# Kernel optimization log

Measured on AMD Instinct MI355X. Metric: run time of the kernel, lower is better.

## Reference

```python
import jax, jax.numpy as jnp
import numpy as np

B, WIN, NN, NF, NH, NOUT = 4, 10, 10000, 8, 64, 1
N = B * WIN * NN          # stacked graph nodes
E = 3200000               # edges
EPS = 1e-5                # BatchNorm eps


def _gcn(x, edge_index, ew, W, b):
    # PyG GCNConv: linear first, then sym-normalized aggregation with self loops.
    xl = x @ W  # [N, H]
    loop = jnp.arange(N)
    row = jnp.concatenate([edge_index[0], loop])
    col = jnp.concatenate([edge_index[1], loop])
    w = jnp.concatenate([ew, jnp.ones((N,), ew.dtype)])
    deg = jax.ops.segment_sum(w, col, num_segments=N)
    dinv = jnp.where(deg > 0, jax.lax.rsqrt(deg), 0.0)
    norm = dinv[row] * w * dinv[col]
    out = jax.ops.segment_sum(norm[:, None] * xl[row], col, num_segments=N)
    return out + b


def _bn(x, g, bta):
    # training-mode BatchNorm1d (batch statistics, biased variance)
    m = x.mean(0)
    v = x.var(0)
    return (x - m) * jax.lax.rsqrt(v + EPS) * g + bta


def _lstm(xs, wih, whh, bih, bhh):
    # xs: [T, Bn, D]; PyTorch gate order i, f, g, o
    H = whh.shape[1]
    Bn = xs.shape[1]
    h0 = jnp.zeros((Bn, H), xs.dtype)
    c0 = jnp.zeros((Bn, H), xs.dtype)
    def step(carry, xt):
        h, c = carry
        gates = xt @ wih.T + bih + h @ whh.T + bhh
        i, f, g, o = jnp.split(gates, 4, axis=-1)
        c = jax.nn.sigmoid(f) * c + jax.nn.sigmoid(i) * jnp.tanh(g)
        h = jax.nn.sigmoid(o) * jnp.tanh(c)
        return (h, c), h
    (hn, cn), ys = jax.lax.scan(step, (h0, c0), xs)
    return ys, hn


def setup_inputs() -> dict:
    key = jax.random.key(0)
    ks = jax.random.split(key, 16)
    def rn(k, shape, s=0.05):
        return jax.random.normal(k, shape, jnp.float32) * s
    return {
        "x": jax.random.normal(ks[0], (N, NF), jnp.float32),
        "edge_index": jax.random.randint(ks[1], (2, E), 0, N),
        "edge_weight": jax.random.uniform(ks[2], (E,), jnp.float32),
        "c1_w": rn(ks[3], (NF, NH)), "c1_b": jnp.zeros((NH,), jnp.float32),
        "c2_w": rn(ks[4], (NH, NH)), "c2_b": jnp.zeros((NH,), jnp.float32),
        "bn1_g": jnp.ones((NH,), jnp.float32), "bn1_b": jnp.zeros((NH,), jnp.float32),
        "bn2_g": jnp.ones((NH,), jnp.float32), "bn2_b": jnp.zeros((NH,), jnp.float32),
        "l1_wih": rn(ks[5], (4 * NH, 2 * NH)), "l1_whh": rn(ks[6], (4 * NH, NH)),
        "l1_bih": jnp.zeros((4 * NH,), jnp.float32), "l1_bhh": jnp.zeros((4 * NH,), jnp.float32),
        "l2_wih": rn(ks[7], (4 * NH, NH)), "l2_whh": rn(ks[8], (4 * NH, NH)),
        "l2_bih": jnp.zeros((4 * NH,), jnp.float32), "l2_bhh": jnp.zeros((4 * NH,), jnp.float32),
        "fc1_w": rn(ks[9], (NH, 2 * NH + WIN * NF)), "fc1_b": jnp.zeros((NH,), jnp.float32),
        "fc2_w": rn(ks[10], (NOUT, NH)), "fc2_b": jnp.zeros((NOUT,), jnp.float32),
    }


def reference(x, edge_index, edge_weight, c1_w, c1_b, c2_w, c2_b,
              bn1_g, bn1_b, bn2_g, bn2_b,
              l1_wih, l1_whh, l1_bih, l1_bhh,
              l2_wih, l2_whh, l2_bih, l2_bhh,
              fc1_w, fc1_b, fc2_w, fc2_b):
    # skip connection: raw features per (batch,node) over the window
    skip = x.reshape(B, WIN, NN, NF).transpose(0, 2, 1, 3).reshape(B * NN, WIN * NF)
    # two GCN layers (dropout is identity in deterministic/eval reference)
    h1 = _bn(jax.nn.relu(_gcn(x, edge_index, edge_weight, c1_w, c1_b)), bn1_g, bn1_b)
    h2 = _bn(jax.nn.relu(_gcn(h1, edge_index, edge_weight, c2_w, c2_b)), bn2_g, bn2_b)
    xc = jnp.concatenate([h1, h2], axis=1)  # [N, 2H]
    xr = xc.reshape(B, WIN, NN, 2 * NH).transpose(1, 0, 2, 3).reshape(WIN, B * NN, 2 * NH)
    ys1, hn1 = _lstm(xr, l1_wih, l1_whh, l1_bih, l1_bhh)
    ys2, hn2 = _lstm(ys1, l2_wih, l2_whh, l2_bih, l2_bhh)
    z = jnp.concatenate([hn1, hn2, skip], axis=1)
    z = jax.nn.relu(z @ fc1_w.T + fc1_b)
    z = jax.nn.relu(z @ fc2_w.T + fc2_b)
    return z.reshape(-1)
```

## Files before the change

### kernel.cpp

```cpp
#include <hip/hip_runtime.h>
#include <math.h>

constexpr int BB     = 4;
constexpr int WINN   = 10;
constexpr int NNODES = 10000;
constexpr int NFEAT  = 8;
constexpr int NHID   = 64;
constexpr int NTOT   = BB * WINN * NNODES;
constexpr int NEDGE  = 3200000;
constexpr int NBN    = BB * NNODES;
constexpr float EPSBN = 1e-5f;

#define DEVFN static __device__ __forceinline__

typedef float f4 __attribute__((ext_vector_type(4)));
typedef short s8v __attribute__((ext_vector_type(8)));
typedef unsigned short ushort_t;
typedef unsigned int uint_t;

DEVFN float sigmoidf_(float x) { return 1.0f / (1.0f + __expf(-x)); }
DEVFN float tanhf_(float x) { return 2.0f / (1.0f + __expf(-2.0f * x)) - 1.0f; }
DEVFN ushort_t f2bf(float f) {
    uint_t x = __float_as_uint(f);
    return (ushort_t)((x + 0x7FFFu + ((x >> 16) & 1u)) >> 16);
}
DEVFN float bf2f(ushort_t u) { return __uint_as_float(((uint_t)u) << 16); }

__global__ void k_diag(float* out, float wsz, int n) {
    int i = blockIdx.x * 256 + threadIdx.x;
    if (i < n) out[i] = wsz;
}

__global__ void k_init(int* cntP, float* sums) {
    int i = blockIdx.x * 256 + threadIdx.x;
    if (i < 8 * NTOT) cntP[i] = 0;
    if (i < 2048) sums[i] = 0.f;
}

__global__ void k_hist(const int* __restrict__ ei, int* __restrict__ cntP) {
    int e = blockIdx.x * 256 + threadIdx.x;
    int p = blockIdx.x & 7;
    if (e < NEDGE) atomicAdd(&cntP[p * NTOT + ei[NEDGE + e]], 1);
}

__global__ void k_scan1(const int* __restrict__ cntP, int* __restrict__ ptr, int* __restrict__ tmp) {
    __shared__ int sdat[256];
    int tid = threadIdx.x;
    int base = blockIdx.x * 1024 + tid * 4;
    int v[4];
#pragma unroll
    for (int j = 0; j < 4; ++j) {
        int idx = base + j;
        int s = 0;
        if (idx < NTOT) {
#pragma unroll
            for (int p = 0; p < 8; ++p) s += cntP[p * NTOT + idx];
        }
        v[j] = s;
    }
    int sum = v[0] + v[1] + v[2] + v[3];
    sdat[tid] = sum;
    __syncthreads();
    for (int ofs = 1; ofs < 256; ofs <<= 1) {
        int x = (tid >= ofs) ? sdat[tid - ofs] : 0;
        __syncthreads();
        sdat[tid] += x;
        __syncthreads();
    }
    int run = sdat[tid] - sum;
    if (base + 0 < NTOT) ptr[base + 0] = run; run += v[0];
    if (base + 1 < NTOT) ptr[base + 1] = run; run += v[1];
    if (base + 2 < NTOT) ptr[base + 2] = run; run += v[2];
    if (base + 3 < NTOT) ptr[base + 3] = run;
    if (tid == 255) tmp[blockIdx.x] = sdat[255];
}

__global__ void k_scan2(int* tmp, int nb) {
    __shared__ int st[512];
    int tid = threadIdx.x;
    int v = (tid < nb) ? tmp[tid] : 0;
    st[tid] = v;
    __syncthreads();
    for (int ofs = 1; ofs < 512; ofs <<= 1) {
        int x = (tid >= ofs) ? st[tid - ofs] : 0;
        __syncthreads();
        st[tid] += x;
        __syncthreads();
    }
    if (tid < nb) tmp[tid] = st[tid] - v;
}

__global__ void k_scan3(int* __restrict__ ptr, int* __restrict__ cntP, const int* __restrict__ tmp) {
    int i = blockIdx.x * 256 + threadIdx.x;
    if (i < NTOT) {
        int p0 = ptr[i] + tmp[i >> 10];
        ptr[i] = p0;
        int run = p0;
#pragma unroll
        for (int p = 0; p < 8; ++p) {
            int c = cntP[p * NTOT + i];
            cntP[p * NTOT + i] = run;
            run += c;
        }
    }
    if (i == 0) ptr[NTOT] = NEDGE;
}

__global__ void k_fill(const int* __restrict__ ei, const float* __restrict__ ew,
                       int* __restrict__ cur8, int2* __restrict__ epack) {
    int e = blockIdx.x * 256 + threadIdx.x;
    if (e >= NEDGE) return;
    int p = blockIdx.x & 7;
    int row = ei[e], col = ei[NEDGE + e];
    int pos = atomicAdd(&cur8[p * NTOT + col], 1);
    epack[pos] = make_int2(row, __float_as_int(ew[e]));
}

__global__ void k_degcsr(const int* __restrict__ ptr, const int2* __restrict__ epack,
                         float* __restrict__ dinv) {
    int tid = threadIdx.x;
    int lane = tid & 63;
    int waveg = blockIdx.x * 4 + (tid >> 6);
    int g = lane >> 3, sub = lane & 7;
    int node = waveg * 8 + g;
    int beg = ptr[node], end = ptr[node + 1];
    float s = 0.f;
    for (int e = beg + sub; e < end; e += 8) s += __int_as_float(epack[e].y);
    s += __shfl_xor(s, 1, 64);
    s += __shfl_xor(s, 2, 64);
    s += __shfl_xor(s, 4, 64);
    if (sub == 0) dinv[node] = rsqrtf(1.0f + s);
}

__global__ void k_gather8(const int* __restrict__ ptr, const int2* __restrict__ epack,
                          const float* __restrict__ x, const float* __restrict__ dinv,
                          float* __restrict__ aggX) {
    int tid = threadIdx.x;
    int lane = tid & 63;
    int waveg = blockIdx.x * 4 + (tid >> 6);
    int g = lane >> 3, ch = lane & 7;
    int node = waveg * 8 + g;
    int beg = ptr[node], end = ptr[node + 1];
    float dv = dinv[node];
    float accE = 0.f;
    int e = beg;
    for (; e + 3 < end; e += 4) {
        int2 p0 = epack[e], p1 = epack[e + 1], p2 = epack[e + 2], p3 = epack[e + 3];
        float n0 = dinv[p0.x] * __int_as_float(p0.y);
        float n1 = dinv[p1.x] * __int_as_float(p1.y);
        float n2 = dinv[p2.x] * __int_as_float(p2.y);
        float n3 = dinv[p3.x] * __int_as_float(p3.y);
        accE = fmaf(n0, x[p0.x * 8 + ch], accE);
        accE = fmaf(n1, x[p1.x * 8 + ch], accE);
        accE = fmaf(n2, x[p2.x * 8 + ch], accE);
        accE = fmaf(n3, x[p3.x * 8 + ch], accE);
    }
    for (; e < end; ++e) {
        int2 p = epack[e];
        accE = fmaf(dinv[p.x] * __int_as_float(p.y), x[p.x * 8 + ch], accE);
    }
    aggX[node * 8 + ch] = dv * fmaf(dv, x[node * 8 + ch], accE);
}

__global__ void k_lin1(const float* __restrict__ aggX, const float* __restrict__ W,
                       const float* __restrict__ bias, ushort_t* __restrict__ rbf,
                       float* __restrict__ sums) {
    __shared__ float sW[NFEAT * NHID];
    int tid = threadIdx.x;
    sW[tid] = W[tid];
    sW[tid + 256] = W[tid + 256];
    __syncthreads();
    int c = tid & 63;
    float b = bias[c];
    float s = 0.f, sq = 0.f;
    int stride = gridDim.x * 256;
    for (int i = blockIdx.x * 256 + tid; i < NTOT * 64; i += stride) {
        int n = i >> 6;
        float acc = b;
#pragma unroll
        for (int f = 0; f < NFEAT; ++f) acc = fmaf(aggX[n * NFEAT + f], sW[f * NHID + c], acc);
        acc = acc > 0.f ? acc : 0.f;
        rbf[i] = f2bf(acc);
        s += acc;
        sq = fmaf(acc, acc, sq);
    }
    __shared__ float ls[4][64], lq[4][64];
    int w = tid >> 6;
    ls[w][c] = s; lq[w][c] = sq;
    __syncthreads();
    if (tid < 64) {
        atomicAdd(&sums[tid], ls[0][tid] + ls[1][tid] + ls[2][tid] + ls[3][tid]);
        atomicAdd(&sums[64 + tid], lq[0][tid] + lq[1][tid] + lq[2][tid] + lq[3][tid]);
    }
}

__global__ void k_bn_final(const float* __restrict__ sums, const float* __restrict__ g,
                           const float* __restrict__ b, float* __restrict__ ss) {
    int i = threadIdx.x;
    if (i >= 64) return;
    float mean = sums[i] * (1.0f / NTOT);
    float var = sums[64 + i] * (1.0f / NTOT) - mean * mean;
    float sc = g[i] * rsqrtf(var + EPSBN);
    ss[i] = sc;
    ss[64 + i] = b[i] - mean * sc;
}

__global__ void k_bn_final8(const float* __restrict__ sums8, const float* __restrict__ g,
                            const float* __restrict__ b, float* __restrict__ ss) {
    int i = threadIdx.x;
    if (i >= 64) return;
    float S = 0.f, Q = 0.f;
#pragma unroll
    for (int m = 0; m < 8; ++m) { S += sums8[m * 128 + i]; Q += sums8[m * 128 + 64 + i]; }
    float mean = S * (1.0f / NTOT);
    float var = Q * (1.0f / NTOT) - mean * mean;
    float sc = g[i] * rsqrtf(var + EPSBN);
    ss[i] = sc;
    ss[64 + i] = b[i] - mean * sc;
}

__global__ void k_gather64b(const int* __restrict__ ptr, const int2* __restrict__ epack,
                            const ushort_t* __restrict__ rbf, const float* __restrict__ dinv,
                            const float* __restrict__ ss1, ushort_t* __restrict__ gout) {
    int lane = threadIdx.x & 63;
    int node = blockIdx.x * 4 + (threadIdx.x >> 6);
    int beg = ptr[node], end = ptr[node + 1];
    float dv = dinv[node];
    float accE = 0.f, accS = 0.f;
    int e = beg;
    for (; e + 3 < end; e += 4) {
        int2 p0 = epack[e], p1 = epack[e + 1], p2 = epack[e + 2], p3 = epack[e + 3];
        float n0 = dinv[p0.x] * __int_as_float(p0.y);
        float n1 = dinv[p1.x] * __int_as_float(p1.y);
        float n2 = dinv[p2.x] * __int_as_float(p2.y);
        float n3 = dinv[p3.x] * __int_as_float(p3.y);
        accE = fmaf(n0, bf2f(rbf[(size_t)p0.x * 64 + lane]), accE);
        accE = fmaf(n1, bf2f(rbf[(size_t)p1.x * 64 + lane]), accE);
        accE = fmaf(n2, bf2f(rbf[(size_t)p2.x * 64 + lane]), accE);
        accE = fmaf(n3, bf2f(rbf[(size_t)p3.x * 64 + lane]), accE);
        accS += n0 + n1 + n2 + n3;
    }
    for (; e < end; ++e) {
        int2 p = epack[e];
        float nv = dinv[p.x] * __int_as_float(p.y);
        accE = fmaf(nv, bf2f(rbf[(size_t)p.x * 64 + lane]), accE);
        accS += nv;
    }
    float G = dv * fmaf(dv, bf2f(rbf[(size_t)node * 64 + lane]), accE);
    float S = dv * (dv + accS);
    gout[(size_t)node * 64 + lane] = f2bf(fmaf(ss1[lane], G, ss1[64 + lane] * S));
}

__global__ void k_lin2c(const ushort_t* __restrict__ gin, const float* __restrict__ W2,
                        const float* __restrict__ bias, ushort_t* __restrict__ dst,
                        float* __restrict__ sums8) {
    __shared__ __align__(16) float srow[4][64];
    __shared__ float ls[4][64], lq[4][64];
    int lane = threadIdx.x & 63, wv = threadIdx.x >> 6;
    float wc[64];
#pragma unroll
    for (int h = 0; h < 64; ++h) wc[h] = W2[h * 64 + lane];
    float b = bias[lane];
    float s = 0.f, sq = 0.f;
    int wid = blockIdx.x * 4 + wv;
    int nw = gridDim.x * 4;
    for (int row = wid; row < NTOT; row += nw) {
        srow[wv][lane] = bf2f(gin[(size_t)row * 64 + lane]);
        float acc = b;
#pragma unroll
        for (int h4 = 0; h4 < 16; ++h4) {
            float4 iv = *reinterpret_cast<const float4*>(&srow[wv][h4 * 4]);
            acc = fmaf(iv.x, wc[h4 * 4 + 0], acc);
            acc = fmaf(iv.y, wc[h4 * 4 + 1], acc);
            acc = fmaf(iv.z, wc[h4 * 4 + 2], acc);
            acc = fmaf(iv.w, wc[h4 * 4 + 3], acc);
        }
        acc = acc > 0.f ? acc : 0.f;
        dst[(size_t)row * 64 + lane] = f2bf(acc);
        s += acc;
        sq = fmaf(acc, acc, sq);
    }
    ls[wv][lane] = s; lq[wv][lane] = sq;
    __syncthreads();
    if (threadIdx.x < 64) {
        float S = ls[0][lane] + ls[1][lane] + ls[2][lane] + ls[3][lane];
        float Q = lq[0][lane] + lq[1][lane] + lq[2][lane] + lq[3][lane];
        float* d = sums8 + (blockIdx.x & 7) * 128;
        atomicAdd(&d[lane], S);
        atomicAdd(&d[64 + lane], Q);
    }
}

__global__ void k_prep(const float* __restrict__ wih1, const float* __restrict__ whh1,
                       const float* __restrict__ bih1, const float* __restrict__ bhh1,
                       const float* __restrict__ wih2, const float* __restrict__ whh2,
                       const float* __restrict__ bih2, const float* __restrict__ bhh2,
                       const float* __restrict__ fc1w,
                       float* wB1f, float* b1, ushort_t* wB2h, float* b2, float* fc1T) {
    int i = blockIdx.x * 256 + threadIdx.x;
    if (i < 256 * 192) {
        int n = i / 192, k = i - n * 192;
        wB1f[i] = (k < 128) ? wih1[n * 128 + k] : whh1[n * 64 + (k - 128)];
    }
    if (i < 256 * 128) {
        int n = i >> 7, k = i & 127;
        wB2h[i] = f2bf((k < 64) ? wih2[n * 64 + k] : whh2[n * 64 + (k - 64)]);
    }
    if (i < 208 * 64) {
        int k = i >> 6, o = i & 63;
        fc1T[i] = fc1w[o * 208 + k];
    }
    if (i < 256) { b1[i] = bih1[i] + bhh1[i]; b2[i] = bih2[i] + bhh2[i]; }
}

__global__ void k_fold2(float* __restrict__ wB1f, float* __restrict__ b1,
                        const float* __restrict__ ss1, const float* __restrict__ ss2,
                        ushort_t* __restrict__ wB1h) {
    int n = threadIdx.x;
    float acc = 0.f;
#pragma unroll
    for (int m = 0; m < 64; ++m) {
        float w = wB1f[n * 192 + m];
        acc = fmaf(w, ss1[64 + m], acc);
        wB1f[n * 192 + m] = w * ss1[m];
    }
#pragma unroll
    for (int m = 0; m < 64; ++m) {
        float w = wB1f[n * 192 + 64 + m];
        acc = fmaf(w, ss2[64 + m], acc);
        wB1f[n * 192 + 64 + m] = w * ss2[m];
    }
    b1[n] += acc;
    __syncthreads();
    for (int j = n; j < 256 * 192; j += 256) wB1h[j] = f2bf(wB1f[j]);
}

__global__ __launch_bounds__(256, 2) void k_lstm_mfma4(
    const ushort_t* __restrict__ h1bf, const ushort_t* __restrict__ h2bf,
    const ushort_t* __restrict__ wB1, const ushort_t* __restrict__ wB2,
    const float* __restrict__ bs1, const float* __restrict__ bs2,
    float* __restrict__ hA, float* __restrict__ hB) {
    __shared__ ushort_t hx1[2][1024], hx2[2][1024];
    int tid = threadIdx.x;
    int lane = tid & 63, wv = tid >> 6;
    int c15 = lane & 15, g4 = lane >> 4;
    int g8 = g4 * 8;
    int bn0 = blockIdx.x * 16;
    int b = bn0 / NNODES, nn0 = bn0 - b * NNODES;

    for (int i = tid; i < 2048; i += 256) {
        if (i < 1024) ((uint_t*)hx1)[i] = 0u;
        else ((uint_t*)hx2)[i - 1024] = 0u;
    }

    s8v w1f[4][6], w2f[4][4];
#pragma unroll
    for (int j = 0; j < 4; ++j) {
        const ushort_t* base1 = wB1 + (size_t)((wv + 4 * j) * 16 + c15) * 192 + g8;
#pragma unroll
        for (int kk = 0; kk < 6; ++kk) w1f[j][kk] = *(const s8v*)(base1 + kk * 32);
        const ushort_t* base2 = wB2 + (size_t)((wv + 4 * j) * 16 + c15) * 128 + g8;
#pragma unroll
        for (int kk = 0; kk < 4; ++kk) w2f[j][kk] = *(const s8v*)(base2 + kk * 32);
    }
    float bi1[4], bi2[4];
#pragma unroll
    for (int j = 0; j < 4; ++j) {
        bi1[j] = bs1[(wv + 4 * j) * 16 + c15];
        bi2[j] = bs2[(wv + 4 * j) * 16 + c15];
    }
    float cA[4], cB[4];
#pragma unroll
    for (int q = 0; q < 4; ++q) { cA[q] = 0.f; cB[q] = 0.f; }

    int r7 = c15 & 7;
    int a_lo = c15 * 64 + ((g4 ^ r7) << 3);
    int a_hi = c15 * 64 + (((4 + g4) ^ r7) << 3);
    int u = wv * 16 + c15;
    int hxcol_hi = (u >> 3) << 3;
    int u7 = u & 7;

    __syncthreads();

    for (int t = 0; t < WINN; ++t) {
        int cur = t & 1, prv = 1 - cur;
        size_t node = (size_t)((b * WINN + t) * NNODES + nn0 + c15) * 64 + g8;
        s8v a[6];
        a[0] = *(const s8v*)(h1bf + node);
        a[1] = *(const s8v*)(h1bf + node + 32);
        a[2] = *(const s8v*)(h2bf + node);
        a[3] = *(const s8v*)(h2bf + node + 32);
        a[4] = *(const s8v*)(&hx1[prv][a_lo]);
        a[5] = *(const s8v*)(&hx1[prv][a_hi]);

        f4 acc[4];
#pragma unroll
        for (int j = 0; j < 4; ++j) { f4 v = {bi1[j], bi1[j], bi1[j], bi1[j]}; acc[j] = v; }
#pragma unroll
        for (int j = 0; j < 4; ++j)
#pragma unroll
            for (int kk = 0; kk < 6; ++kk)
                acc[j] = __builtin_amdgcn_mfma_f32_16x16x32_bf16(a[kk], w1f[j][kk], acc[j], 0, 0, 0);
#pragma unroll
        for (int q = 0; q < 4; ++q) {
            float ig = sigmoidf_(acc[0][q]);
            float fg = sigmoidf_(acc[1][q]);
            float gg = tanhf_(acc[2][q]);
            float og = sigmoidf_(acc[3][q]);
            float cv = fmaf(fg, cA[q], ig * gg);
            cA[q] = cv;
            float hv = og * tanhf_(cv);
            int rr = g4 * 4 + q;
            hx1[cur][rr * 64 + (hxcol_hi ^ ((rr & 7) << 3)) + u7] = f2bf(hv);
        }
        __syncthreads();

        s8v r[4];
        r[0] = *(const s8v*)(&hx1[cur][a_lo]);
        r[1] = *(const s8v*)(&hx1[cur][a_hi]);
        r[2] = *(const s8v*)(&hx2[prv][a_lo]);
        r[3] = *(const s8v*)(&hx2[prv][a_hi]);
#pragma unroll
        for (int j = 0; j < 4; ++j) { f4 v = {bi2[j], bi2[j], bi2[j], bi2[j]}; acc[j] = v; }
#pragma unroll
        for (int j = 0; j < 4; ++j)
#pragma unroll
            for (int kk = 0; kk < 4; ++kk)
                acc[j] = __builtin_amdgcn_mfma_f32_16x16x32_bf16(r[kk], w2f[j][kk], acc[j], 0, 0, 0);
#pragma unroll
        for (int q = 0; q < 4; ++q) {
            float ig = sigmoidf_(acc[0][q]);
            float fg = sigmoidf_(acc[1][q]);
            float gg = tanhf_(acc[2][q]);
            float og = sigmoidf_(acc[3][q]);
            float cv = fmaf(fg, cB[q], ig * gg);
            cB[q] = cv;
            float hv = og * tanhf_(cv);
            int rr = g4 * 4 + q;
            hx2[cur][rr * 64 + (hxcol_hi ^ ((rr & 7) << 3)) + u7] = f2bf(hv);
        }
    }
    __syncthreads();
    int fin = (WINN - 1) & 1;
    for (int i = tid; i < 1024; i += 256) {
        int rr = i >> 6, uu = i & 63;
        int hw2 = rr * 64 + ((((uu >> 3) ^ (rr & 7)) << 3)) + (uu & 7);
        hA[(size_t)(bn0 + rr) * 64 + uu] = bf2f(hx1[fin][hw2]);
        hB[(size_t)(bn0 + rr) * 64 + uu] = bf2f(hx2[fin][hw2]);
    }
}

__global__ void k_head(const float* __restrict__ hA, const float* __restrict__ hB,
                       const float* __restrict__ x, const float* __restrict__ fc1T,
                       const float* __restrict__ fc1b, const float* __restrict__ fc2w,
                       const float* __restrict__ fc2b, float* __restrict__ out) {
    int lane = threadIdx.x & 63, wv = threadIdx.x >> 6;
    int bn = blockIdx.x * 4 + wv;
    __shared__ float sz[4][208];
    int b = bn / NNODES, nn = bn - b * NNODES;
    for (int k = lane; k < 208; k += 64) {
        float v;
        if (k < 64) v = hA[(size_t)bn * 64 + k];
        else if (k < 128) v = hB[(size_t)bn * 64 + (k - 64)];
        else {
            int kk = k - 128;
            int w = kk >> 3, f = kk & 7;
            v = x[(size_t)((b * WINN + w) * NNODES + nn) * NFEAT + f];
        }
        sz[wv][k] = v;
    }
    __syncthreads();
    float acc = fc1b[lane];
    for (int k = 0; k < 208; ++k) acc = fmaf(sz[wv][k], fc1T[k * 64 + lane], acc);
    acc = acc > 0.f ? acc : 0.f;
    float v = acc * fc2w[lane];
#pragma unroll
    for (int m = 32; m >= 1; m >>= 1) v += __shfl_xor(v, m, 64);
    if (lane == 0) {
        float z = v + fc2b[0];
        out[bn] = z > 0.f ? z : 0.f;
    }
}

extern "C" void kernel_launch(void* const* d_in, const int* in_sizes, int n_in,
                              void* d_out, int out_size, void* d_ws, size_t ws_size,
                              hipStream_t stream) {
    const float* x     = (const float*)d_in[0];
    const int*   ei    = (const int*)d_in[1];
    const float* ew    = (const float*)d_in[2];
    const float* c1w   = (const float*)d_in[3];
    const float* c1b   = (const float*)d_in[4];
    const float* c2w   = (const float*)d_in[5];
    const float* c2b   = (const float*)d_in[6];
    const float* bn1g  = (const float*)d_in[7];
    const float* bn1b  = (const float*)d_in[8];
    const float* bn2g  = (const float*)d_in[9];
    const float* bn2b  = (const float*)d_in[10];
    const float* wih1  = (const float*)d_in[11];
    const float* whh1  = (const float*)d_in[12];
    const float* bih1  = (const float*)d_in[13];
    const float* bhh1  = (const float*)d_in[14];
    const float* wih2  = (const float*)d_in[15];
    const float* whh2  = (const float*)d_in[16];
    const float* bih2  = (const float*)d_in[17];
    const float* bhh2  = (const float*)d_in[18];
    const float* fc1w  = (const float*)d_in[19];
    const float* fc1b  = (const float*)d_in[20];
    const float* fc2w  = (const float*)d_in[21];
    const float* fc2b  = (const float*)d_in[22];
    float* out = (float*)d_out;

    float* ws = (float*)d_ws;
    size_t off = 0;
    auto A = [&](size_t n) { float* p = ws + off; off += n; return p; };
    float* dinv   = A(NTOT);
    float* aggX   = A((size_t)NTOT * NFEAT);
    ushort_t* h1bf = (ushort_t*)A((size_t)NTOT * 32);
    ushort_t* h2bf = (ushort_t*)A((size_t)NTOT * 32);
    ushort_t* gbuf = (ushort_t*)A((size_t)NTOT * 32);

    size_t uoff = off;
    float* hA = A((size_t)NBN * 64);
    float* hB = A((size_t)NBN * 64);
    A(2 * (size_t)NEDGE + (NTOT + 1) + 8 * (size_t)NTOT - 2 * (size_t)NBN * 64);
    int2* epack = (int2*)(ws + uoff);
    int*  ptr   = (int*)(epack + NEDGE);
    int*  cntP  = ptr + NTOT + 1;

    float* wB1f = A(256 * 192);
    ushort_t* wB1h = (ushort_t*)A(256 * 96);
    ushort_t* wB2h = (ushort_t*)A(256 * 64);
    float* b1   = A(256);
    float* b2   = A(256);
    float* fc1T = A(208 * 64);
    float* sums = A(2048);
    float* ss1  = A(128);
    float* ss2  = A(128);
    float* scanTmpF = A(512);
    int* scanTmp = (int*)scanTmpF;

    if (ws_size < off * sizeof(float)) {
        k_diag<<<(out_size + 255) / 256, 256, 0, stream>>>(out, (float)ws_size, out_size);
        return;
    }

    constexpr int SCAN_NB = (NTOT + 1023) / 1024;

    k_init<<<8 * NTOT / 256, 256, 0, stream>>>(cntP, sums);
    k_hist<<<NEDGE / 256, 256, 0, stream>>>(ei, cntP);
    k_scan1<<<SCAN_NB, 256, 0, stream>>>(cntP, ptr, scanTmp);
    k_scan2<<<1, 512, 0, stream>>>(scanTmp, SCAN_NB);
    k_scan3<<<(NTOT + 255) / 256, 256, 0, stream>>>(ptr, cntP, scanTmp);
    k_fill<<<NEDGE / 256, 256, 0, stream>>>(ei, ew, cntP, epack);
    k_degcsr<<<NTOT / 8 / 4, 256, 0, stream>>>(ptr, epack, dinv);
    k_prep<<<192, 256, 0, stream>>>(wih1, whh1, bih1, bhh1, wih2, whh2, bih2, bhh2,
                                    fc1w, wB1f, b1, wB2h, b2, fc1T);

    k_gather8<<<NTOT / 8 / 4, 256, 0, stream>>>(ptr, epack, x, dinv, aggX);
    k_lin1<<<512, 256, 0, stream>>>(aggX, c1w, c1b, h1bf, sums);
    k_bn_final<<<1, 64, 0, stream>>>(sums, bn1g, bn1b, ss1);

    k_gather64b<<<NTOT / 4, 256, 0, stream>>>(ptr, epack, h1bf, dinv, ss1, gbuf);
    k_lin2c<<<2048, 256, 0, stream>>>(gbuf, c2w, c2b, h2bf, sums + 128);
    k_bn_final8<<<1, 64, 0, stream>>>(sums + 128, bn2g, bn2b, ss2);
    k_fold2<<<1, 256, 0, stream>>>(wB1f, b1, ss1, ss2, wB1h);

    k_lstm_mfma4<<<NBN / 16, 256, 0, stream>>>(h1bf, h2bf, wB1h, wB2h, b1, b2, hA, hB);

    k_head<<<NBN / 4, 256, 0, stream>>>(hA, hB, x, fc1T, fc1b, fc2w, fc2b, out);
}
```

Before: 1.116 ms.

## Build CSR via partition-major staging then regroup, and prefetch LSTM inputs

CSR construction now scans the 8 partition counters in partition-major order, so each partition's edges land in a contiguous staging array through atomics that stay local to that partition. A second pass then copies each node's per-partition segments into the final node-major CSR. This is meant to make the atomic scatter more local, at the cost of an extra scan pass, an extra 3.2M-edge copy and a larger workspace. Separately, the LSTM kernel prefetches the next timestep's h1/h2 inputs from global memory during the current step to hide load latency.

```diff
diff --git a/kernel.cpp b/kernel.cpp
--- a/kernel.cpp
+++ b/kernel.cpp
@@ -31,19 +31,19 @@
     if (i < n) out[i] = wsz;
 }
 
-__global__ void k_init(int* cntP, float* sums) {
+__global__ void k_init(int* cnt8, float* sums) {
     int i = blockIdx.x * 256 + threadIdx.x;
-    if (i < 8 * NTOT) cntP[i] = 0;
+    if (i < 8 * NTOT) cnt8[i] = 0;
     if (i < 2048) sums[i] = 0.f;
 }
 
-__global__ void k_hist(const int* __restrict__ ei, int* __restrict__ cntP) {
+__global__ void k_hist(const int* __restrict__ ei, int* __restrict__ cnt8) {
     int e = blockIdx.x * 256 + threadIdx.x;
     int p = blockIdx.x & 7;
-    if (e < NEDGE) atomicAdd(&cntP[p * NTOT + ei[NEDGE + e]], 1);
-}
-
-__global__ void k_scan1(const int* __restrict__ cntP, int* __restrict__ ptr, int* __restrict__ tmp) {
+    if (e < NEDGE) atomicAdd(&cnt8[p * NTOT + ei[NEDGE + e]], 1);
+}
+
+__global__ void k_scan1(const int* __restrict__ cnt8, int* __restrict__ ptr, int* __restrict__ tmp) {
     __shared__ int sdat[256];
     int tid = threadIdx.x;
     int base = blockIdx.x * 1024 + tid * 4;
@@ -54,7 +54,7 @@
         int s = 0;
         if (idx < NTOT) {
 #pragma unroll
-            for (int p = 0; p < 8; ++p) s += cntP[p * NTOT + idx];
+            for (int p = 0; p < 8; ++p) s += cnt8[p * NTOT + idx];
         }
         v[j] = s;
     }
@@ -76,44 +76,96 @@
 }
 
 __global__ void k_scan2(int* tmp, int nb) {
-    __shared__ int st[512];
-    int tid = threadIdx.x;
-    int v = (tid < nb) ? tmp[tid] : 0;
-    st[tid] = v;
-    __syncthreads();
-    for (int ofs = 1; ofs < 512; ofs <<= 1) {
+    __shared__ int st[256];
+    int tid = threadIdx.x;
+    int per = (nb + 255) / 256;
+    int s = 0;
+#pragma unroll 4
+    for (int k = 0; k < per; ++k) {
+        int idx = tid * per + k;
+        if (idx < nb) s += tmp[idx];
+    }
+    st[tid] = s;
+    __syncthreads();
+    for (int ofs = 1; ofs < 256; ofs <<= 1) {
         int x = (tid >= ofs) ? st[tid - ofs] : 0;
         __syncthreads();
         st[tid] += x;
         __syncthreads();
     }
-    if (tid < nb) tmp[tid] = st[tid] - v;
-}
-
-__global__ void k_scan3(int* __restrict__ ptr, int* __restrict__ cntP, const int* __restrict__ tmp) {
+    int run = st[tid] - s;
+    for (int k = 0; k < per; ++k) {
+        int idx = tid * per + k;
+        if (idx < nb) { int v = tmp[idx]; tmp[idx] = run; run += v; }
+    }
+}
+
+__global__ void k_scan3(int* __restrict__ ptr, const int* __restrict__ tmp) {
     int i = blockIdx.x * 256 + threadIdx.x;
-    if (i < NTOT) {
-        int p0 = ptr[i] + tmp[i >> 10];
-        ptr[i] = p0;
-        int run = p0;
-#pragma unroll
-        for (int p = 0; p < 8; ++p) {
-            int c = cntP[p * NTOT + i];
-            cntP[p * NTOT + i] = run;
-            run += c;
-        }
-    }
+    if (i < NTOT) ptr[i] += tmp[i >> 10];
     if (i == 0) ptr[NTOT] = NEDGE;
 }
 
-__global__ void k_fill(const int* __restrict__ ei, const float* __restrict__ ew,
-                       int* __restrict__ cur8, int2* __restrict__ epack) {
+__global__ void k_scan1p(const int* __restrict__ cnt8, int* __restrict__ ptr8, int* __restrict__ tmpP) {
+    __shared__ int sdat[256];
+    int tid = threadIdx.x;
+    int base = blockIdx.x * 1024 + tid * 4;
+    int v0 = cnt8[base], v1 = cnt8[base + 1], v2 = cnt8[base + 2], v3 = cnt8[base + 3];
+    int sum = v0 + v1 + v2 + v3;
+    sdat[tid] = sum;
+    __syncthreads();
+    for (int ofs = 1; ofs < 256; ofs <<= 1) {
+        int x = (tid >= ofs) ? sdat[tid - ofs] : 0;
+        __syncthreads();
+        sdat[tid] += x;
+        __syncthreads();
+    }
+    int run = sdat[tid] - sum;
+    ptr8[base] = run; run += v0;
+    ptr8[base + 1] = run; run += v1;
+    ptr8[base + 2] = run; run += v2;
+    ptr8[base + 3] = run;
+    if (tid == 255) tmpP[blockIdx.x] = sdat[255];
+}
+
+__global__ void k_scan3p(int* __restrict__ ptr8, int* __restrict__ cur8, const int* __restrict__ tmpP) {
+    int i = blockIdx.x * 256 + threadIdx.x;
+    if (i < 8 * NTOT) {
+        int v = ptr8[i] + tmpP[i >> 10];
+        ptr8[i] = v;
+        cur8[i] = v;
+    }
+}
+
+__global__ void k_fillA(const int* __restrict__ ei, const float* __restrict__ ew,
+                        int* __restrict__ cur8, int2* __restrict__ epackP) {
     int e = blockIdx.x * 256 + threadIdx.x;
     if (e >= NEDGE) return;
     int p = blockIdx.x & 7;
     int row = ei[e], col = ei[NEDGE + e];
     int pos = atomicAdd(&cur8[p * NTOT + col], 1);
-    epack[pos] = make_int2(row, __float_as_int(ew[e]));
+    epackP[pos] = make_int2(row, __float_as_int(ew[e]));
+}
+
+__global__ void k_fillB(const int* __restrict__ ptr8, const int* __restrict__ cur8,
+                        const int* __restrict__ ptr, const int2* __restrict__ epackP,
+                        int2* __restrict__ epack) {
+    int tid = threadIdx.x;
+    int lane = tid & 63;
+    int waveg = blockIdx.x * 4 + (tid >> 6);
+    int g = lane >> 3, p = lane & 7;
+    int node = waveg * 8 + g;
+    int beg = ptr8[p * NTOT + node];
+    int cnt = cur8[p * NTOT + node] - beg;
+    int pfx = cnt;
+#pragma unroll
+    for (int ofs = 1; ofs < 8; ofs <<= 1) {
+        int o = __shfl_up(pfx, ofs, 8);
+        if (p >= ofs) pfx += o;
+    }
+    pfx -= cnt;
+    int dst = ptr[node] + pfx;
+    for (int k = 0; k < cnt; ++k) epack[dst + k] = epackP[beg + k];
 }
 
 __global__ void k_degcsr(const int* __restrict__ ptr, const int2* __restrict__ epack,
@@ -380,27 +432,38 @@
     int hxcol_hi = (u >> 3) << 3;
     int u7 = u & 7;
 
+    size_t nd0 = (size_t)((b * WINN + 0) * NNODES + nn0 + c15) * 64 + g8;
+    s8v g0 = *(const s8v*)(h1bf + nd0);
+    s8v g1 = *(const s8v*)(h1bf + nd0 + 32);
+    s8v g2 = *(const s8v*)(h2bf + nd0);
+    s8v g3 = *(const s8v*)(h2bf + nd0 + 32);
+
     __syncthreads();
 
     for (int t = 0; t < WINN; ++t) {
         int cur = t & 1, prv = 1 - cur;
-        size_t node = (size_t)((b * WINN + t) * NNODES + nn0 + c15) * 64 + g8;
-        s8v a[6];
-        a[0] = *(const s8v*)(h1bf + node);
-        a[1] = *(const s8v*)(h1bf + node + 32);
-        a[2] = *(const s8v*)(h2bf + node);
-        a[3] = *(const s8v*)(h2bf + node + 32);
-        a[4] = *(const s8v*)(&hx1[prv][a_lo]);
-        a[5] = *(const s8v*)(&hx1[prv][a_hi]);
+        int tn = (t + 1 < WINN) ? t + 1 : t;
+        size_t ndn = (size_t)((b * WINN + tn) * NNODES + nn0 + c15) * 64 + g8;
+        s8v n0 = *(const s8v*)(h1bf + ndn);
+        s8v n1 = *(const s8v*)(h1bf + ndn + 32);
+        s8v n2 = *(const s8v*)(h2bf + ndn);
+        s8v n3 = *(const s8v*)(h2bf + ndn + 32);
+
+        s8v a4 = *(const s8v*)(&hx1[prv][a_lo]);
+        s8v a5 = *(const s8v*)(&hx1[prv][a_hi]);
 
         f4 acc[4];
 #pragma unroll
         for (int j = 0; j < 4; ++j) { f4 v = {bi1[j], bi1[j], bi1[j], bi1[j]}; acc[j] = v; }
 #pragma unroll
-        for (int j = 0; j < 4; ++j)
-#pragma unroll
-            for (int kk = 0; kk < 6; ++kk)
-                acc[j] = __builtin_amdgcn_mfma_f32_16x16x32_bf16(a[kk], w1f[j][kk], acc[j], 0, 0, 0);
+        for (int j = 0; j < 4; ++j) {
+            acc[j] = __builtin_amdgcn_mfma_f32_16x16x32_bf16(g0, w1f[j][0], acc[j], 0, 0, 0);
+            acc[j] = __builtin_amdgcn_mfma_f32_16x16x32_bf16(g1, w1f[j][1], acc[j], 0, 0, 0);
+            acc[j] = __builtin_amdgcn_mfma_f32_16x16x32_bf16(g2, w1f[j][2], acc[j], 0, 0, 0);
+            acc[j] = __builtin_amdgcn_mfma_f32_16x16x32_bf16(g3, w1f[j][3], acc[j], 0, 0, 0);
+            acc[j] = __builtin_amdgcn_mfma_f32_16x16x32_bf16(a4, w1f[j][4], acc[j], 0, 0, 0);
+            acc[j] = __builtin_amdgcn_mfma_f32_16x16x32_bf16(a5, w1f[j][5], acc[j], 0, 0, 0);
+        }
 #pragma unroll
         for (int q = 0; q < 4; ++q) {
             float ig = sigmoidf_(acc[0][q]);
@@ -415,18 +478,19 @@
         }
         __syncthreads();
 
-        s8v r[4];
-        r[0] = *(const s8v*)(&hx1[cur][a_lo]);
-        r[1] = *(const s8v*)(&hx1[cur][a_hi]);
-        r[2] = *(const s8v*)(&hx2[prv][a_lo]);
-        r[3] = *(const s8v*)(&hx2[prv][a_hi]);
+        s8v r0 = *(const s8v*)(&hx1[cur][a_lo]);
+        s8v r1 = *(const s8v*)(&hx1[cur][a_hi]);
+        s8v r2 = *(const s8v*)(&hx2[prv][a_lo]);
+        s8v r3 = *(const s8v*)(&hx2[prv][a_hi]);
 #pragma unroll
         for (int j = 0; j < 4; ++j) { f4 v = {bi2[j], bi2[j], bi2[j], bi2[j]}; acc[j] = v; }
 #pragma unroll
-        for (int j = 0; j < 4; ++j)
-#pragma unroll
-            for (int kk = 0; kk < 4; ++kk)
-                acc[j] = __builtin_amdgcn_mfma_f32_16x16x32_bf16(r[kk], w2f[j][kk], acc[j], 0, 0, 0);
+        for (int j = 0; j < 4; ++j) {
+            acc[j] = __builtin_amdgcn_mfma_f32_16x16x32_bf16(r0, w2f[j][0], acc[j], 0, 0, 0);
+            acc[j] = __builtin_amdgcn_mfma_f32_16x16x32_bf16(r1, w2f[j][1], acc[j], 0, 0, 0);
+            acc[j] = __builtin_amdgcn_mfma_f32_16x16x32_bf16(r2, w2f[j][2], acc[j], 0, 0, 0);
+            acc[j] = __builtin_amdgcn_mfma_f32_16x16x32_bf16(r3, w2f[j][3], acc[j], 0, 0, 0);
+        }
 #pragma unroll
         for (int q = 0; q < 4; ++q) {
             float ig = sigmoidf_(acc[0][q]);
@@ -439,6 +503,7 @@
             int rr = g4 * 4 + q;
             hx2[cur][rr * 64 + (hxcol_hi ^ ((rr & 7) << 3)) + u7] = f2bf(hv);
         }
+        g0 = n0; g1 = n1; g2 = n2; g3 = n3;
     }
     __syncthreads();
     int fin = (WINN - 1) & 1;
@@ -522,10 +587,13 @@
     size_t uoff = off;
     float* hA = A((size_t)NBN * 64);
     float* hB = A((size_t)NBN * 64);
-    A(2 * (size_t)NEDGE + (NTOT + 1) + 8 * (size_t)NTOT - 2 * (size_t)NBN * 64);
-    int2* epack = (int2*)(ws + uoff);
-    int*  ptr   = (int*)(epack + NEDGE);
-    int*  cntP  = ptr + NTOT + 1;
+    size_t csr_ints = 2 * (size_t)NEDGE + (NTOT + 2) + 2 * (size_t)NEDGE + 8 * (size_t)NTOT + 8 * (size_t)NTOT;
+    A(csr_ints - 2 * (size_t)NBN * 64);
+    int2* epack  = (int2*)(ws + uoff);
+    int*  ptr    = (int*)(epack + NEDGE);
+    int2* epackP = (int2*)(ptr + NTOT + 2);
+    int*  ptr8   = (int*)(epackP + NEDGE);
+    int*  cur8   = ptr8 + 8 * NTOT;
 
     float* wB1f = A(256 * 192);
     ushort_t* wB1h = (ushort_t*)A(256 * 96);
@@ -536,7 +604,7 @@
     float* sums = A(2048);
     float* ss1  = A(128);
     float* ss2  = A(128);
-    float* scanTmpF = A(512);
+    float* scanTmpF = A(4096);
     int* scanTmp = (int*)scanTmpF;
 
     if (ws_size < off * sizeof(float)) {
@@ -544,14 +612,20 @@
         return;
     }
 
-    constexpr int SCAN_NB = (NTOT + 1023) / 1024;
-
-    k_init<<<8 * NTOT / 256, 256, 0, stream>>>(cntP, sums);
-    k_hist<<<NEDGE / 256, 256, 0, stream>>>(ei, cntP);
-    k_scan1<<<SCAN_NB, 256, 0, stream>>>(cntP, ptr, scanTmp);
-    k_scan2<<<1, 512, 0, stream>>>(scanTmp, SCAN_NB);
-    k_scan3<<<(NTOT + 255) / 256, 256, 0, stream>>>(ptr, cntP, scanTmp);
-    k_fill<<<NEDGE / 256, 256, 0, stream>>>(ei, ew, cntP, epack);
+    constexpr int SCAN_NB  = (NTOT + 1023) / 1024;
+    constexpr int SCAN_NBP = (8 * NTOT) / 1024;
+
+    int* cnt8 = cur8;
+    k_init<<<8 * NTOT / 256, 256, 0, stream>>>(cnt8, sums);
+    k_hist<<<NEDGE / 256, 256, 0, stream>>>(ei, cnt8);
+    k_scan1<<<SCAN_NB, 256, 0, stream>>>(cnt8, ptr, scanTmp);
+    k_scan2<<<1, 256, 0, stream>>>(scanTmp, SCAN_NB);
+    k_scan3<<<(NTOT + 255) / 256, 256, 0, stream>>>(ptr, scanTmp);
+    k_scan1p<<<SCAN_NBP, 256, 0, stream>>>(cnt8, ptr8, scanTmp);
+    k_scan2<<<1, 256, 0, stream>>>(scanTmp, SCAN_NBP);
+    k_scan3p<<<(8 * NTOT + 255) / 256, 256, 0, stream>>>(ptr8, cur8, scanTmp);
+    k_fillA<<<NEDGE / 256, 256, 0, stream>>>(ei, ew, cur8, epackP);
+    k_fillB<<<NTOT / 32, 256, 0, stream>>>(ptr8, cur8, ptr, epackP, epack);
     k_degcsr<<<NTOT / 8 / 4, 256, 0, stream>>>(ptr, epack, dinv);
     k_prep<<<192, 256, 0, stream>>>(wih1, whh1, bih1, bhh1, wih2, whh2, bih2, bhh2,
                                     fc1w, wB1f, b1, wB2h, b2, fc1T);
```

New measurement: 1.150 ms. +3.1%, slower.
